# Optimization experiments

Measured on AMD Instinct MI355X. Metric: run time of the kernel, lower is better.

The kernel has to match this reference:

```python
import jax, jax.numpy as jnp
import numpy as np

FEAT_STRIDE = 8
SCALES = (4.0, 8.0, 16.0)
RATIOS = (0.5, 1.0, 2.0)
A = len(SCALES) * len(RATIOS)          # 9 anchors per location
PRE_NMS = 2048
POST_NMS = 300
NMS_THRESH = 0.7


def _gen_base_anchors():
    # cube anchors at scale*stride, ratio applied to depth; boxes (x1,y1,z1,x2,y2,z2)
    base = float(FEAT_STRIDE)
    ctr = (base - 1.0) / 2.0
    boxes = []
    for r in RATIOS:
        for s in SCALES:
            w = h = base * s
            d = base * s * r
            boxes.append([ctr - 0.5 * (w - 1), ctr - 0.5 * (h - 1), ctr - 0.5 * (d - 1),
                          ctr + 0.5 * (w - 1), ctr + 0.5 * (h - 1), ctr + 0.5 * (d - 1)])
    return jnp.asarray(boxes, jnp.float32)  # [A,6]


def _all_anchors(D, H, W):
    sz = jnp.arange(D, dtype=jnp.float32) * FEAT_STRIDE
    sy = jnp.arange(H, dtype=jnp.float32) * FEAT_STRIDE
    sx = jnp.arange(W, dtype=jnp.float32) * FEAT_STRIDE
    zz, yy, xx = jnp.meshgrid(sz, sy, sx, indexing='ij')  # order (d,h,w) matches score layout
    shifts = jnp.stack([xx, yy, zz, xx, yy, zz], -1).reshape(-1, 6)  # [K,6]
    return (shifts[:, None, :] + _gen_base_anchors()[None]).reshape(-1, 6)  # [K*A,6]


def _apply_deltas(anchors, deltas):
    w = anchors[:, 3] - anchors[:, 0] + 1.0
    h = anchors[:, 4] - anchors[:, 1] + 1.0
    d = anchors[:, 5] - anchors[:, 2] + 1.0
    cx = anchors[:, 0] + 0.5 * w
    cy = anchors[:, 1] + 0.5 * h
    cz = anchors[:, 2] + 0.5 * d
    dx, dy, dz, dw, dh, dd = [deltas[:, i] for i in range(6)]
    pcx = dx * w + cx; pcy = dy * h + cy; pcz = dz * d + cz
    pw = jnp.exp(dw) * w; ph = jnp.exp(dh) * h; pd = jnp.exp(dd) * d
    return jnp.stack([pcx - 0.5 * pw, pcy - 0.5 * ph, pcz - 0.5 * pd,
                      pcx + 0.5 * pw, pcy + 0.5 * ph, pcz + 0.5 * pd], -1)


def _clip_boxes(boxes, iminfo):  # iminfo = [D_im, H_im, W_im]
    lo = jnp.zeros((6,), boxes.dtype)
    hi = jnp.stack([iminfo[2], iminfo[1], iminfo[0], iminfo[2], iminfo[1], iminfo[0]]) - 1.0
    return jnp.clip(boxes, lo[None, :], hi[None, :])


def _pairwise_iou3d(b):  # b: [N,6]
    lo = jnp.maximum(b[:, None, :3], b[None, :, :3])          # [N,N,3]
    hi = jnp.minimum(b[:, None, 3:], b[None, :, 3:])
    inter = jnp.prod(jnp.clip(hi - lo + 1.0, 0.0), axis=-1)   # [N,N]
    vol = jnp.prod(b[:, 3:] - b[:, :3] + 1.0, axis=-1)        # [N]
    return inter / (vol[:, None] + vol[None, :] - inter)


def _nms_keep(iou):
    N = iou.shape[0]
    idx = jnp.arange(N)
    def body(i, keep):
        sup = (iou[i] > NMS_THRESH) & keep[i] & (idx > i)
        return keep & ~sup
    return jax.lax.fori_loop(0, N, body, jnp.ones((N,), bool))


def _propose_one(scores, deltas, anchors, iminfo):
    boxes = _clip_boxes(_apply_deltas(anchors, deltas), iminfo)  # [KA,6]
    _, order = jax.lax.top_k(scores, PRE_NMS)
    b = boxes[order]                                             # [PRE,6], score-sorted desc
    keep = _nms_keep(_pairwise_iou3d(b))
    key = jnp.where(keep, jnp.arange(PRE_NMS), PRE_NMS)
    sel = jnp.argsort(key)[:POST_NMS]                            # first POST_NMS kept, in score order
    valid = (key[sel] < PRE_NMS).astype(b.dtype)
    return b[sel] * valid[:, None]                               # zero-padded rows if < POST_NMS kept


def _forward(base_feat, im_info, W_conv, b_conv, W_cls, b_cls, W_bbox, b_bbox):
    B, C, D, H, W = base_feat.shape
    x = jax.lax.conv_general_dilated(
        base_feat, W_conv, (1, 1, 1), ((1, 1), (1, 1), (1, 1)),
        dimension_numbers=('NCDHW', 'OIDHW', 'NCDHW'))
    x = jax.nn.relu(x + b_conv[None, :, None, None, None])       # [B,512,D,H,W]
    cls = jnp.einsum('bcdhw,oc->bodhw', x, W_cls) + b_cls[None, :, None, None, None]
    prob = jax.nn.softmax(cls.reshape(B, 2, A, D, H, W), axis=1)  # reshape(x,2) + softmax(dim=1)
    fg = prob[:, 1]                                               # [B,A,D,H,W]
    scores = jnp.transpose(fg, (0, 2, 3, 4, 1)).reshape(B, -1)    # [B, K*A], order (d,h,w,a)
    bb = jnp.einsum('bcdhw,oc->bodhw', x, W_bbox) + b_bbox[None, :, None, None, None]
    deltas = jnp.transpose(bb.reshape(B, A, 6, D, H, W), (0, 3, 4, 5, 1, 2)).reshape(B, -1, 6)
    anchors = _all_anchors(D, H, W)
    rois6 = jax.vmap(lambda s, d, im: _propose_one(s, d, anchors, im))(scores, deltas, im_info)
    bidx = jnp.broadcast_to(jnp.arange(B, dtype=rois6.dtype)[:, None, None], (B, POST_NMS, 1))
    return jnp.concatenate([bidx, rois6], -1)                     # [B, POST_NMS, 7]


def setup_inputs() -> dict:
    key = jax.random.key(0)
    ks = jax.random.split(key, 4)
    B, din, D, H, W = 2, 128, 8, 32, 32
    base_feat = jax.random.normal(ks[0], (B, din, D, H, W), jnp.float32)
    im_info = jnp.asarray([[64.0, 256.0, 256.0]] * B, jnp.float32)  # (D_im, H_im, W_im)
    gt_boxes = jnp.zeros((B, 20, 7), jnp.float32)
    num_boxes = jnp.zeros((B,), jnp.int64)
    W_conv = jax.random.normal(ks[1], (512, din, 3, 3, 3), jnp.float32) * 0.02
    b_conv = jnp.zeros((512,), jnp.float32)
    W_cls = jax.random.normal(ks[2], (2 * A, 512), jnp.float32) * 0.01
    b_cls = jnp.zeros((2 * A,), jnp.float32)
    W_bbox = jax.random.normal(ks[3], (6 * A, 512), jnp.float32) * 0.01
    b_bbox = jnp.zeros((6 * A,), jnp.float32)
    return {"base_feat": base_feat, "im_info": im_info, "gt_boxes": gt_boxes,
            "num_boxes": num_boxes, "W_conv": W_conv, "b_conv": b_conv,
            "W_cls": W_cls, "b_cls": b_cls, "W_bbox": W_bbox, "b_bbox": b_bbox}


def reference(base_feat, im_info, gt_boxes, num_boxes, W_conv, b_conv, W_cls, b_cls, W_bbox, b_bbox):
    # Eval-mode RPN forward: losses are 0 in the original; gt_boxes/num_boxes unused.
    rois = _forward(base_feat, im_info, W_conv, b_conv, W_cls, b_cls, W_bbox, b_bbox)
    return rois
```

## Files before the change

kernel.cpp:

```cpp
#include <hip/hip_runtime.h>
#include <stdint.h>

#define BATCH 2
#define CIN 128
#define COUT 512
#define DD 8
#define PSPAT 8192
#define NA 9
#define NANCH 73728
#define PRE 2048
#define POST 300
#define CAP 4096
#define NMS_TH 0.7f

typedef unsigned short u16;
typedef _Float16 f16x8 __attribute__((ext_vector_type(8)));
typedef float f32x16 __attribute__((ext_vector_type(16)));
typedef unsigned int uint32x4 __attribute__((ext_vector_type(4)));

constexpr size_t OFF_WT   = 0;
constexpr size_t OFF_WHT  = 7077888;
constexpr size_t OFF_X    = 7241728;
constexpr size_t OFF_SC   = 40796160;
constexpr size_t OFF_BX   = 41385984;
constexpr size_t OFF_SB   = 44957696;
constexpr size_t OFF_MK   = 45056000;
constexpr size_t OFF_HIST = 16;
constexpr size_t OFF_CAND = 524304;

#define NT_WT   (27 * 128 * 512)
#define NT_WHT  (512 * 80)
__global__ void k_wtrans(const float* __restrict__ Wc, u16* __restrict__ Wg,
                         const float* __restrict__ Wcls, const float* __restrict__ Wbb,
                         float* __restrict__ Wht) {
    int e = blockIdx.x * blockDim.x + threadIdx.x;
    if (e < NT_WT) {
        const int k    = e & 63;
        const int n    = (e >> 6) & 127;
        const int half = (e >> 13) & 1;
        const int rest = e >> 14;
        const int co = (rest / 27) * 128 + n;
        const int ci = half * 64 + k;
        const int tp = rest % 27;
        const float v = Wc[(co * 128 + ci) * 27 + tp] * 1024.f;
        const _Float16 h = (_Float16)v;
        const _Float16 l = (_Float16)(v - (float)h);
        char* rb = (char*)Wg + (((size_t)(rest * 2 + half)) << 15) + n * 256;
        const int hcol = (k >> 3) ^ (n & 15);
        const int lcol = ((k >> 3) | 8) ^ (n & 15);
        const int kb = (k & 7) << 1;
        *(u16*)(rb + (hcol << 4) + kb) = __builtin_bit_cast(unsigned short, h);
        *(u16*)(rb + (lcol << 4) + kb) = __builtin_bit_cast(unsigned short, l);
        return;
    }
    e -= NT_WT;
    if (e >= NT_WHT) return;
    int q = e % 80;
    int c = e / 80;
    int og = q / 10, k = q % 10;
    int o = og * 9 + k;
    float v = 0.f;
    if (k < 9) v = (o < 18) ? Wcls[o * 512 + c] : Wbb[(o - 18) * 512 + c];
    Wht[e] = v;
}

#define MFMA(A, B, C) __builtin_amdgcn_mfma_f32_32x32x16_f16((A), (B), (C), 0, 0, 0)
#define Z16 {0.f,0.f,0.f,0.f,0.f,0.f,0.f,0.f,0.f,0.f,0.f,0.f,0.f,0.f,0.f,0.f}

#define PK2(YA, YB, UH, UL) { \
    const float sa_ = (YA) * 1024.f, sb_ = (YB) * 1024.f; \
    const _Float16 ha_ = (_Float16)sa_, hb_ = (_Float16)sb_; \
    const _Float16 la_ = (_Float16)(sa_ - (float)ha_); \
    const _Float16 lb_ = (_Float16)(sb_ - (float)hb_); \
    UH = (unsigned)__builtin_bit_cast(unsigned short, ha_) | \
         ((unsigned)__builtin_bit_cast(unsigned short, hb_) << 16); \
    UL = (unsigned)__builtin_bit_cast(unsigned short, la_) | \
         ((unsigned)__builtin_bit_cast(unsigned short, lb_) << 16); }

#define BLDI(N, KK) { \
    const int h2_ = hb_ + (N); \
    const bool ok_ = okw_ && ((unsigned)h2_ < 32u); \
    const float* ap_ = in + (((size_t)(cb0_ + ((KK) << 4))) << 13) + spo_ + (h2_ << 5); \
    y[N][KK][0] = ok_ ? ap_[0]     : 0.f; \
    y[N][KK][1] = ok_ ? ap_[8192]  : 0.f; \
    y[N][KK][2] = ok_ ? ap_[16384] : 0.f; \
    y[N][KK][3] = ok_ ? ap_[24576] : 0.f; \
    y[N][KK][4] = ok_ ? ap_[32768] : 0.f; \
    y[N][KK][5] = ok_ ? ap_[40960] : 0.f; \
    y[N][KK][6] = ok_ ? ap_[49152] : 0.f; \
    y[N][KK][7] = ok_ ? ap_[57344] : 0.f; }

#define ALOADISS(S) { \
    const int tap_ = t0 + ((S) >> 1); \
    const int kd_ = tap_ / 9, kh_ = (tap_ / 3) % 3, kw_ = tap_ % 3; \
    const int id_ = d0 + kd_ - 1; \
    const int w2_ = l31 + kw_ - 1; \
    const bool okw_ = (unsigned)w2_ < 32u; \
    const int hb_ = h0 + (wn << 1) + kh_ - 1; \
    const int cb0_ = b * CIN + (((S) & 1) << 6) + (cq << 3); \
    const long long spo_ = ((long long)id_ << 10) + w2_; \
    BLDI(0, 0) BLDI(0, 1) BLDI(0, 2) BLDI(0, 3) \
    BLDI(1, 0) BLDI(1, 1) BLDI(1, 2) BLDI(1, 3) }

#define CVTFRAG(N, KK, BH, BL) { \
    unsigned uh0_, uh1_, uh2_, uh3_, ul0_, ul1_, ul2_, ul3_; \
    PK2(y[N][KK][0], y[N][KK][1], uh0_, ul0_) \
    PK2(y[N][KK][2], y[N][KK][3], uh1_, ul1_) \
    PK2(y[N][KK][4], y[N][KK][5], uh2_, ul2_) \
    PK2(y[N][KK][6], y[N][KK][7], uh3_, ul3_) \
    { uint32x4 th_ = {uh0_, uh1_, uh2_, uh3_}; BH = __builtin_bit_cast(f16x8, th_); } \
    { uint32x4 tl_ = {ul0_, ul1_, ul2_, ul3_}; BL = __builtin_bit_cast(f16x8, tl_); } }

#define CVTALL() { \
    CVTFRAG(0, 0, bh00, bl00) CVTFRAG(0, 1, bh01, bl01) \
    CVTFRAG(0, 2, bh02, bl02) CVTFRAG(0, 3, bh03, bl03) \
    CVTFRAG(1, 0, bh10, bl10) CVTFRAG(1, 1, bh11, bl11) \
    CVTFRAG(1, 2, bh12, bl12) CVTFRAG(1, 3, bh13, bl13) }

#define WISSUE(S, BUF) { \
    const int tap_ = t0 + ((S) >> 1); \
    const char* gw_ = WgB + (((size_t)((nt * 27 + tap_) * 2 + ((S) & 1))) << 15) \
                    + (wv << 13) + ln16; \
    char* lb_ = smem + ((BUF) << 15) + (wv << 13); \
    _Pragma("unroll") \
    for (int j_ = 0; j_ < 8; ++j_) \
        __builtin_amdgcn_global_load_lds( \
            (const __attribute__((address_space(1))) void*)(gw_ + (j_ << 10)), \
            (__attribute__((address_space(3))) void*)(lb_ + (j_ << 10)), 16, 0, 0); }

#define KKSTEP(KK, BH0, BL0, BH1, BL1) { \
    const int ch_ = ((((KK) << 1) + cq) ^ rsw) << 4; \
    const int cl_ = (((((KK) << 1) + cq) | 8) ^ rsw) << 4; \
    const char* r0_ = wb_ + (rm0 << 8); \
    const char* r1_ = wb_ + (rm1 << 8); \
    const f16x8 wh0 = *(const f16x8*)(r0_ + ch_); \
    const f16x8 wl0 = *(const f16x8*)(r0_ + cl_); \
    const f16x8 wh1 = *(const f16x8*)(r1_ + ch_); \
    const f16x8 wl1 = *(const f16x8*)(r1_ + cl_); \
    acc00 = MFMA(wh0, BH0, acc00); acc00 = MFMA(wh0, BL0, acc00); acc00 = MFMA(wl0, BH0, acc00); \
    acc01 = MFMA(wh0, BH1, acc01); acc01 = MFMA(wh0, BL1, acc01); acc01 = MFMA(wl0, BH1, acc01); \
    acc10 = MFMA(wh1, BH0, acc10); acc10 = MFMA(wh1, BL0, acc10); acc10 = MFMA(wl1, BH0, acc10); \
    acc11 = MFMA(wh1, BH1, acc11); acc11 = MFMA(wh1, BL1, acc11); acc11 = MFMA(wl1, BH1, acc11); }

#define COMPUTE(BUF) { \
    const char* wb_ = smem + ((BUF) << 15); \
    KKSTEP(0, bh00, bl00, bh10, bl10) \
    KKSTEP(1, bh01, bl01, bh11, bl11) \
    KKSTEP(2, bh02, bl02, bh12, bl12) \
    KKSTEP(3, bh03, bl03, bh13, bl13) }

#define EPI(ACC, MI, NI) { \
    const int coB_ = co0 + (wm << 6) + ((MI) << 5) + hl4; \
    const int pt_  = p0 + (wn << 6) + ((NI) << 5) + l31; \
    _Pragma("unroll") \
    for (int g_ = 0; g_ < 4; ++g_) { \
        _Pragma("unroll") \
        for (int q_ = 0; q_ < 4; ++q_) { \
            const int co_ = coB_ + (g_ << 3) + q_; \
            const float v_ = ACC[g_ * 4 + q_] * 9.5367431640625e-07f + bconv[co_]; \
            x[((size_t)((b << 9) + co_) << 13) + pt_] = fmaxf(v_, 0.f); \
        } } }

__global__ __launch_bounds__(256, 2) void k_conv(const float* __restrict__ in,
                                                 const u16* __restrict__ Wg,
                                                 const float* __restrict__ bconv,
                                                 float* __restrict__ x) {
    __shared__ __align__(16) char smem[65536];
    const int tid  = threadIdx.x;
    const int bx   = blockIdx.x;
    const int nt   = blockIdx.y;
    const int b    = blockIdx.z;
    const int p0   = bx << 7;
    const int d0   = bx >> 3;
    const int h0   = (bx & 7) << 2;
    const int co0  = nt << 7;

    const int lane = tid & 63;
    const int wv   = tid >> 6;
    const int wm   = wv & 1;
    const int wn   = wv >> 1;
    const int l31  = lane & 31;
    const int cq   = lane >> 5;
    const int hl4  = cq << 2;
    const int rsw  = l31 & 15;
    const int rm0  = (wm << 6) + l31;
    const int rm1  = rm0 + 32;
    const int ln16 = lane << 4;

    const int t0   = (d0 == 0) ? 9 : 0;
    const int nTap = 27 - (((d0 == 0) || (d0 == 7)) ? 9 : 0);
    const int NS   = nTap * 2;

    const char* WgB = (const char*)Wg;

    float y[2][4][8];
    f16x8 bh00, bh01, bh02, bh03, bh10, bh11, bh12, bh13;
    f16x8 bl00, bl01, bl02, bl03, bl10, bl11, bl12, bl13;
    f32x16 acc00 = Z16, acc01 = Z16, acc10 = Z16, acc11 = Z16;

    WISSUE(0, 0)
    ALOADISS(0)
    __syncthreads();

    for (int s = 0; s < NS; ++s) {
        if (s + 1 < NS) { WISSUE(s + 1, (s + 1) & 1) }
        CVTALL()
        __builtin_amdgcn_sched_barrier(0);
        if (s + 1 < NS) { ALOADISS(s + 1) }
        __builtin_amdgcn_sched_barrier(0);
        COMPUTE(s & 1)
        __syncthreads();
    }

    EPI(acc00, 0, 0)
    EPI(acc01, 0, 1)
    EPI(acc10, 1, 0)
    EPI(acc11, 1, 1)
}

__global__ __launch_bounds__(256) void k_heads(const float* __restrict__ x,
                                               const float* __restrict__ Wht,
                                               const float* __restrict__ bcls,
                                               const float* __restrict__ bbb,
                                               const float* __restrict__ iminfo,
                                               float* __restrict__ scores,
                                               float* __restrict__ boxes,
                                               unsigned int* __restrict__ hist) {
    __shared__ __align__(16) float smx[4096];
    __shared__ __align__(16) float Whs[2560];
    __shared__ __align__(16) float ex[10240];
    const int tid = threadIdx.x;
    const int p0  = blockIdx.x * 128;
    const int b   = blockIdx.y;
    const int pl  = tid & 31;
    const int og  = tid >> 5;

    float acc[4][9] = {};

    for (int cc = 0; cc < 512; cc += 32) {
        __syncthreads();
        #pragma unroll
        for (int i = 0; i < 4; ++i) {
            int e4 = tid + i * 256;
            int ch = e4 >> 5;
            int pt4 = (e4 & 31) * 4;
            *(float4*)&smx[ch * 128 + pt4] =
                *(const float4*)&x[((size_t)(b * COUT + cc + ch) << 13) + p0 + pt4];
        }
        #pragma unroll
        for (int i = 0; i < 10; ++i) {
            int e = tid + i * 256;
            Whs[e] = Wht[cc * 80 + e];
        }
        __syncthreads();
        for (int kk = 0; kk < 32; ++kk) {
            float4 a4 = *(const float4*)&smx[kk * 128 + pl * 4];
            const float* wp = &Whs[kk * 80 + og * 10];
            float2 w0 = *(const float2*)(wp);
            float2 w1 = *(const float2*)(wp + 2);
            float2 w2 = *(const float2*)(wp + 4);
            float2 w3 = *(const float2*)(wp + 6);
            float  w8 = wp[8];
            float wv[9] = {w0.x, w0.y, w1.x, w1.y, w2.x, w2.y, w3.x, w3.y, w8};
            #pragma unroll
            for (int k = 0; k < 9; ++k) {
                float wk = wv[k];
                acc[0][k] += a4.x * wk;
                acc[1][k] += a4.y * wk;
                acc[2][k] += a4.z * wk;
                acc[3][k] += a4.w * wk;
            }
        }
    }

    __syncthreads();
    #pragma unroll
    for (int pi = 0; pi < 4; ++pi)
        #pragma unroll
        for (int k = 0; k < 9; ++k)
            ex[(pl * 4 + pi) * 80 + og * 10 + k] = acc[pi][k];
    __syncthreads();

    if (tid < 128) {
        const int p = p0 + tid;
        float v[72];
        #pragma unroll
        for (int og2 = 0; og2 < 8; ++og2)
            #pragma unroll
            for (int k = 0; k < 9; ++k)
                v[og2 * 9 + k] = ex[tid * 80 + og2 * 10 + k];

        const float im0 = iminfo[b * 3 + 0], im1 = iminfo[b * 3 + 1], im2 = iminfo[b * 3 + 2];
        const float hix = im2 - 1.f, hiy = im1 - 1.f, hiz = im0 - 1.f;
        const int d = p >> 10, h = (p >> 5) & 31, w = p & 31;
        const float sx = w * 8.f, sy = h * 8.f, sz = d * 8.f;

        #pragma unroll 1
        for (int a = 0; a < 9; ++a) {
            float c0 = v[a] + bcls[a];
            float c1 = v[9 + a] + bcls[9 + a];
            float m  = fmaxf(c0, c1);
            float e0 = expf(c0 - m), e1 = expf(c1 - m);
            float sc = e1 / (e0 + e1);
            scores[b * NANCH + p * 9 + a] = sc;
            atomicAdd(&hist[b * 65536 + (__float_as_uint(sc) >> 16)], 1u);

            float aw = (float)(32 << (a % 3));
            float ad = aw * 0.5f * (float)(1 << (a / 3));
            float ax1 = sx + 3.5f - 0.5f * (aw - 1.f);
            float ax2 = sx + 3.5f + 0.5f * (aw - 1.f);
            float ay1 = sy + 3.5f - 0.5f * (aw - 1.f);
            float ay2 = sy + 3.5f + 0.5f * (aw - 1.f);
            float az1 = sz + 3.5f - 0.5f * (ad - 1.f);
            float az2 = sz + 3.5f + 0.5f * (ad - 1.f);
            float ww_ = ax2 - ax1 + 1.f, hh_ = ay2 - ay1 + 1.f, dd_ = az2 - az1 + 1.f;
            float cx = ax1 + 0.5f * ww_, cy = ay1 + 0.5f * hh_, cz = az1 + 0.5f * dd_;

            const float* dv = &v[18 + a * 6];
            float dx = dv[0] + bbb[a * 6 + 0];
            float dy = dv[1] + bbb[a * 6 + 1];
            float dz = dv[2] + bbb[a * 6 + 2];
            float dw = dv[3] + bbb[a * 6 + 3];
            float dh = dv[4] + bbb[a * 6 + 4];
            float dd2 = dv[5] + bbb[a * 6 + 5];
            float pcx = dx * ww_ + cx, pcy = dy * hh_ + cy, pcz = dz * dd_ + cz;
            float pw = expf(dw) * ww_, ph = expf(dh) * hh_, pd = expf(dd2) * dd_;
            float x1 = fminf(fmaxf(pcx - 0.5f * pw, 0.f), hix);
            float y1 = fminf(fmaxf(pcy - 0.5f * ph, 0.f), hiy);
            float z1 = fminf(fmaxf(pcz - 0.5f * pd, 0.f), hiz);
            float x2 = fminf(fmaxf(pcx + 0.5f * pw, 0.f), hix);
            float y2 = fminf(fmaxf(pcy + 0.5f * ph, 0.f), hiy);
            float z2 = fminf(fmaxf(pcz + 0.5f * pd, 0.f), hiz);
            float* bp = &boxes[(size_t)(b * NANCH + p * 9 + a) * 6];
            bp[0] = x1; bp[1] = y1; bp[2] = z1; bp[3] = x2; bp[4] = y2; bp[5] = z2;
        }
    }
}

__global__ __launch_bounds__(1024) void k_cutcompact(const float* __restrict__ scores,
                                                     const unsigned int* __restrict__ hist,
                                                     unsigned long long* __restrict__ cand) {
    __shared__ unsigned int cs[1024], scan[1024];
    __shared__ unsigned int sh_cut, sh_pos;
    const int b = blockIdx.x, tid = threadIdx.x;
    const unsigned int* h = hist + b * 65536;
    unsigned int s = 0;
    for (int i = 0; i < 64; ++i) s += h[tid * 64 + i];
    cs[tid] = s; scan[tid] = s;
    if (tid == 0) sh_pos = 0;
    __syncthreads();
    for (int d = 1; d < 1024; d <<= 1) {
        unsigned int v = scan[tid];
        unsigned int add = (tid + d < 1024) ? scan[tid + d] : 0u;
        __syncthreads();
        scan[tid] = v + add;
        __syncthreads();
    }
    unsigned int above = (tid + 1 < 1024) ? scan[tid + 1] : 0u;
    if (above < PRE && above + cs[tid] >= PRE) {
        unsigned int cum = above;
        for (int x = tid * 64 + 63; x >= tid * 64; --x) {
            cum += h[x];
            if (cum >= PRE) { sh_cut = (unsigned int)x; break; }
        }
    }
    __syncthreads();
    const unsigned int cut = sh_cut;
    const float* sc = scores + b * NANCH;
    for (int i = tid; i < NANCH; i += 1024) {
        unsigned int u = __float_as_uint(sc[i]);
        if ((u >> 16) >= cut) {
            unsigned int pos = atomicAdd(&sh_pos, 1u);
            if (pos < CAP) cand[b * CAP + pos] = ((unsigned long long)(~u) << 32) | (unsigned)i;
        }
    }
    __syncthreads();
    const unsigned int cnt = (sh_pos < CAP) ? sh_pos : CAP;
    for (int i = (int)cnt + tid; i < CAP; i += 1024)
        cand[b * CAP + i] = ~0ull;
}

__global__ __launch_bounds__(1024) void k_sort2(const unsigned long long* __restrict__ cand,
                                                const float* __restrict__ boxes,
                                                float* __restrict__ sboxes) {
    __shared__ unsigned long long sk[CAP];
    const int b = blockIdx.x, tid = threadIdx.x;
    for (int i = tid; i < CAP; i += 1024) sk[i] = cand[b * CAP + i];
    __syncthreads();
    for (int k = 2; k <= CAP; k <<= 1) {
        for (int j = k >> 1; j > 0; j >>= 1) {
            #pragma unroll 1
            for (int i = tid; i < CAP; i += 1024) {
                int ixj = i ^ j;
                if (ixj > i) {
                    unsigned long long va = sk[i], vb = sk[ixj];
                    bool up = ((i & k) == 0);
                    if ((va > vb) == up) { sk[i] = vb; sk[ixj] = va; }
                }
            }
            __syncthreads();
        }
    }
    for (int r = tid; r < PRE; r += 1024) {
        unsigned int n = (unsigned int)(sk[r] & 0xFFFFFFFFull);
        const float* src = &boxes[(size_t)(b * NANCH + (int)n) * 6];
        float* dst = &sboxes[(size_t)(b * PRE + r) * 6];
        #pragma unroll
        for (int c = 0; c < 6; ++c) dst[c] = src[c];
    }
}

__global__ __launch_bounds__(256) void k_mask(const float* __restrict__ sboxes,
                                              unsigned long long* __restrict__ mask) {
    if (blockIdx.y < blockIdx.x) return;
    __shared__ float rb[64 * 6], cb[64 * 6];
    const int i0 = blockIdx.x * 64, j0 = blockIdx.y * 64, b = blockIdx.z;
    const int tid = threadIdx.x;
    for (int e = tid; e < 384; e += 256) {
        rb[e] = sboxes[(size_t)(b * PRE + i0) * 6 + e];
        cb[e] = sboxes[(size_t)(b * PRE + j0) * 6 + e];
    }
    __syncthreads();
    const int wave = tid >> 6, lane = tid & 63;
    const float bx1 = cb[lane * 6 + 0], by1 = cb[lane * 6 + 1], bz1 = cb[lane * 6 + 2];
    const float bx2 = cb[lane * 6 + 3], by2 = cb[lane * 6 + 4], bz2 = cb[lane * 6 + 5];
    const float vb = (bx2 - bx1 + 1.f) * (by2 - by1 + 1.f) * (bz2 - bz1 + 1.f);
    const int j = j0 + lane;
    for (int rr = 0; rr < 16; ++rr) {
        const int il = wave * 16 + rr;
        const int i = i0 + il;
        float ax1 = rb[il * 6 + 0], ay1 = rb[il * 6 + 1], az1 = rb[il * 6 + 2];
        float ax2 = rb[il * 6 + 3], ay2 = rb[il * 6 + 4], az2 = rb[il * 6 + 5];
        float va = (ax2 - ax1 + 1.f) * (ay2 - ay1 + 1.f) * (az2 - az1 + 1.f);
        float ix = fmaxf(fminf(ax2, bx2) - fmaxf(ax1, bx1) + 1.f, 0.f);
        float iy = fmaxf(fminf(ay2, by2) - fmaxf(ay1, by1) + 1.f, 0.f);
        float iz = fmaxf(fminf(az2, bz2) - fmaxf(az1, bz1) + 1.f, 0.f);
        float inter = ix * iy * iz;
        float iou = inter / (va + vb - inter);
        bool bit = (j > i) && (iou > NMS_TH);
        unsigned long long word = __ballot(bit);
        if (lane == 0) mask[(size_t)(b * PRE + i) * 32 + (j0 >> 6)] = word;
    }
}

__global__ __launch_bounds__(64) void k_nms(const unsigned long long* __restrict__ mask,
                                            const float* __restrict__ sboxes,
                                            float* __restrict__ out) {
    const int b = blockIdx.x, lane = threadIdx.x;
    __shared__ int sel[POST];
    unsigned long long keep = ~0ull;
    const int lw = lane & 31;
    const unsigned long long* mrow = mask + (size_t)b * PRE * 32 + lw;
    unsigned long long b0 = mrow[0 * 32], b1 = mrow[1 * 32], b2 = mrow[2 * 32], b3 = mrow[3 * 32];
    unsigned long long b4 = mrow[4 * 32], b5 = mrow[5 * 32], b6 = mrow[6 * 32], b7 = mrow[7 * 32];
    int kcount = 0;

#define NMS_STEP(J, BUF)                                                        \
    {                                                                           \
        int i = i0 + (J);                                                       \
        unsigned long long cur = (lw >= (i >> 6)) ? BUF : 0ull;                 \
        int nr = i0 + 8 + (J);                                                  \
        BUF = (nr < PRE) ? mrow[(size_t)nr * 32] : 0ull;                        \
        unsigned long long kw = __shfl(keep, i >> 6);                           \
        if ((kw >> (i & 63)) & 1ull) {                                          \
            if (lane < 32) keep &= ~cur;                                        \
            if (lane == 0 && kcount < POST) sel[kcount] = i;                    \
            ++kcount;                                                           \
            if (kcount >= POST) goto nms_done;                                  \
        }                                                                       \
    }

    for (int i0 = 0; i0 < PRE; i0 += 8) {
        NMS_STEP(0, b0) NMS_STEP(1, b1) NMS_STEP(2, b2) NMS_STEP(3, b3)
        NMS_STEP(4, b4) NMS_STEP(5, b5) NMS_STEP(6, b6) NMS_STEP(7, b7)
    }
nms_done:
    __syncthreads();
    const int kc = kcount;
    for (int r = lane; r < POST; r += 64) {
        float* op = &out[(size_t)(b * POST + r) * 7];
        op[0] = (float)b;
        if (r < kc) {
            const float* sb = &sboxes[(size_t)(b * PRE + sel[r]) * 6];
            #pragma unroll
            for (int c = 0; c < 6; ++c) op[1 + c] = sb[c];
        } else {
            #pragma unroll
            for (int c = 0; c < 6; ++c) op[1 + c] = 0.f;
        }
    }
#undef NMS_STEP
}

extern "C" void kernel_launch(void* const* d_in, const int* in_sizes, int n_in,
                              void* d_out, int out_size, void* d_ws, size_t ws_size,
                              hipStream_t stream) {
    const float* base_feat = (const float*)d_in[0];
    const float* im_info   = (const float*)d_in[1];
    const float* W_conv    = (const float*)d_in[4];
    const float* b_conv    = (const float*)d_in[5];
    const float* W_cls     = (const float*)d_in[6];
    const float* b_cls     = (const float*)d_in[7];
    const float* W_bbox    = (const float*)d_in[8];
    const float* b_bbox    = (const float*)d_in[9];

    char* ws = (char*)d_ws;
    u16* Wg        = (u16*)(ws + OFF_WT);
    float* Wht     = (float*)(ws + OFF_WHT);
    float* x       = (float*)(ws + OFF_X);
    float* scores  = (float*)(ws + OFF_SC);
    float* boxes   = (float*)(ws + OFF_BX);
    float* sboxes  = (float*)(ws + OFF_SB);
    unsigned long long* mask = (unsigned long long*)(ws + OFF_MK);
    unsigned int* hist = (unsigned int*)(ws + OFF_HIST);
    unsigned long long* cand = (unsigned long long*)(ws + OFF_CAND);

    const int NTRANS = NT_WT + NT_WHT;
    k_wtrans<<<(NTRANS + 255) / 256, 256, 0, stream>>>(W_conv, Wg, W_cls, W_bbox, Wht);
    k_conv<<<dim3(64, 4, 2), 256, 0, stream>>>(base_feat, Wg, b_conv, x);
    hipMemsetAsync(hist, 0, BATCH * 65536 * sizeof(unsigned int), stream);
    k_heads<<<dim3(64, 2), 256, 0, stream>>>(x, Wht, b_cls, b_bbox, im_info, scores, boxes, hist);
    k_cutcompact<<<BATCH, 1024, 0, stream>>>(scores, hist, cand);
    k_sort2<<<BATCH, 1024, 0, stream>>>(cand, boxes, sboxes);
    k_mask<<<dim3(32, 32, 2), 256, 0, stream>>>(sboxes, mask);
    k_nms<<<BATCH, 64, 0, stream>>>(mask, sboxes, (float*)d_out);
}
```

Measured before the change: 650.7 us.

## Pre-split input into channel-last fp16 hi/lo buffers for conv

Adds a pre-pass kernel that transposes the input to a channel-innermost layout and splits it into fp16 high and low halves once. The conv kernel then loads ready f16x8 fragments with vector loads instead of eight strided scalar fp32 loads plus per-fragment conversion, and double-buffers the A operands across steps. This removes the conversion work repeated across the four output-channel tiles and the uncoalesced loads. The cost is an extra launch and extra workspace traffic, and it falls back to the old kernel when the workspace is too small.

```diff
diff --git a/kernel.cpp b/kernel.cpp
--- a/kernel.cpp
+++ b/kernel.cpp
@@ -27,6 +27,9 @@
 constexpr size_t OFF_MK   = 45056000;
 constexpr size_t OFF_HIST = 16;
 constexpr size_t OFF_CAND = 524304;
+constexpr size_t OFF_XH   = 46104576;
+constexpr size_t OFF_XL   = 50298880;
+constexpr size_t WS_NEED_FAST = 54493184;
 
 #define NT_WT   (27 * 128 * 512)
 #define NT_WHT  (512 * 80)
@@ -64,58 +67,35 @@
     Wht[e] = v;
 }
 
+__global__ __launch_bounds__(256) void k_split(const float* __restrict__ in,
+                                               u16* __restrict__ xh, u16* __restrict__ xl) {
+    __shared__ float t[128][33];
+    const int blk = blockIdx.x;
+    const int b = blk >> 8, d = (blk >> 5) & 7, h = blk & 31;
+    const int tid = threadIdx.x;
+    const float* src = in + ((size_t)b << 20) + d * 1024 + h * 32;
+    #pragma unroll
+    for (int i = 0; i < 16; ++i) {
+        const int e = tid + i * 256;
+        const int ci = e >> 5, w = e & 31;
+        t[ci][w] = src[(size_t)ci * 8192 + w];
+    }
+    __syncthreads();
+    const size_t ob = (size_t)((b * 8 + d) * 32 + h) * 4096;
+    #pragma unroll
+    for (int i = 0; i < 16; ++i) {
+        const int e = tid + i * 256;
+        const int w = e >> 7, ci = e & 127;
+        const float v = t[ci][w] * 1024.f;
+        const _Float16 hh = (_Float16)v;
+        const _Float16 ll = (_Float16)(v - (float)hh);
+        xh[ob + w * 128 + ci] = __builtin_bit_cast(unsigned short, hh);
+        xl[ob + w * 128 + ci] = __builtin_bit_cast(unsigned short, ll);
+    }
+}
+
 #define MFMA(A, B, C) __builtin_amdgcn_mfma_f32_32x32x16_f16((A), (B), (C), 0, 0, 0)
 #define Z16 {0.f,0.f,0.f,0.f,0.f,0.f,0.f,0.f,0.f,0.f,0.f,0.f,0.f,0.f,0.f,0.f}
-
-#define PK2(YA, YB, UH, UL) { \
-    const float sa_ = (YA) * 1024.f, sb_ = (YB) * 1024.f; \
-    const _Float16 ha_ = (_Float16)sa_, hb_ = (_Float16)sb_; \
-    const _Float16 la_ = (_Float16)(sa_ - (float)ha_); \
-    const _Float16 lb_ = (_Float16)(sb_ - (float)hb_); \
-    UH = (unsigned)__builtin_bit_cast(unsigned short, ha_) | \
-         ((unsigned)__builtin_bit_cast(unsigned short, hb_) << 16); \
-    UL = (unsigned)__builtin_bit_cast(unsigned short, la_) | \
-         ((unsigned)__builtin_bit_cast(unsigned short, lb_) << 16); }
-
-#define BLDI(N, KK) { \
-    const int h2_ = hb_ + (N); \
-    const bool ok_ = okw_ && ((unsigned)h2_ < 32u); \
-    const float* ap_ = in + (((size_t)(cb0_ + ((KK) << 4))) << 13) + spo_ + (h2_ << 5); \
-    y[N][KK][0] = ok_ ? ap_[0]     : 0.f; \
-    y[N][KK][1] = ok_ ? ap_[8192]  : 0.f; \
-    y[N][KK][2] = ok_ ? ap_[16384] : 0.f; \
-    y[N][KK][3] = ok_ ? ap_[24576] : 0.f; \
-    y[N][KK][4] = ok_ ? ap_[32768] : 0.f; \
-    y[N][KK][5] = ok_ ? ap_[40960] : 0.f; \
-    y[N][KK][6] = ok_ ? ap_[49152] : 0.f; \
-    y[N][KK][7] = ok_ ? ap_[57344] : 0.f; }
-
-#define ALOADISS(S) { \
-    const int tap_ = t0 + ((S) >> 1); \
-    const int kd_ = tap_ / 9, kh_ = (tap_ / 3) % 3, kw_ = tap_ % 3; \
-    const int id_ = d0 + kd_ - 1; \
-    const int w2_ = l31 + kw_ - 1; \
-    const bool okw_ = (unsigned)w2_ < 32u; \
-    const int hb_ = h0 + (wn << 1) + kh_ - 1; \
-    const int cb0_ = b * CIN + (((S) & 1) << 6) + (cq << 3); \
-    const long long spo_ = ((long long)id_ << 10) + w2_; \
-    BLDI(0, 0) BLDI(0, 1) BLDI(0, 2) BLDI(0, 3) \
-    BLDI(1, 0) BLDI(1, 1) BLDI(1, 2) BLDI(1, 3) }
-
-#define CVTFRAG(N, KK, BH, BL) { \
-    unsigned uh0_, uh1_, uh2_, uh3_, ul0_, ul1_, ul2_, ul3_; \
-    PK2(y[N][KK][0], y[N][KK][1], uh0_, ul0_) \
-    PK2(y[N][KK][2], y[N][KK][3], uh1_, ul1_) \
-    PK2(y[N][KK][4], y[N][KK][5], uh2_, ul2_) \
-    PK2(y[N][KK][6], y[N][KK][7], uh3_, ul3_) \
-    { uint32x4 th_ = {uh0_, uh1_, uh2_, uh3_}; BH = __builtin_bit_cast(f16x8, th_); } \
-    { uint32x4 tl_ = {ul0_, ul1_, ul2_, ul3_}; BL = __builtin_bit_cast(f16x8, tl_); } }
-
-#define CVTALL() { \
-    CVTFRAG(0, 0, bh00, bl00) CVTFRAG(0, 1, bh01, bl01) \
-    CVTFRAG(0, 2, bh02, bl02) CVTFRAG(0, 3, bh03, bl03) \
-    CVTFRAG(1, 0, bh10, bl10) CVTFRAG(1, 1, bh11, bl11) \
-    CVTFRAG(1, 2, bh12, bl12) CVTFRAG(1, 3, bh13, bl13) }
 
 #define WISSUE(S, BUF) { \
     const int tap_ = t0 + ((S) >> 1); \
@@ -142,13 +122,6 @@
     acc10 = MFMA(wh1, BH0, acc10); acc10 = MFMA(wh1, BL0, acc10); acc10 = MFMA(wl1, BH0, acc10); \
     acc11 = MFMA(wh1, BH1, acc11); acc11 = MFMA(wh1, BL1, acc11); acc11 = MFMA(wl1, BH1, acc11); }
 
-#define COMPUTE(BUF) { \
-    const char* wb_ = smem + ((BUF) << 15); \
-    KKSTEP(0, bh00, bl00, bh10, bl10) \
-    KKSTEP(1, bh01, bl01, bh11, bl11) \
-    KKSTEP(2, bh02, bl02, bh12, bl12) \
-    KKSTEP(3, bh03, bl03, bh13, bl13) }
-
 #define EPI(ACC, MI, NI) { \
     const int coB_ = co0 + (wm << 6) + ((MI) << 5) + hl4; \
     const int pt_  = p0 + (wn << 6) + ((NI) << 5) + l31; \
@@ -160,6 +133,156 @@
             const float v_ = ACC[g_ * 4 + q_] * 9.5367431640625e-07f + bconv[co_]; \
             x[((size_t)((b << 9) + co_) << 13) + pt_] = fmaxf(v_, 0.f); \
         } } }
+
+#define FLD(N, KK, BH, BL) { \
+    const int h2_ = hb_ + (N); \
+    const bool ok_ = okw_ && ((unsigned)h2_ < 32u); \
+    const size_t ix_ = sbase_ + ((size_t)((h2_ & 31) << 5) << 7); \
+    const f16x8 vh_ = *(const f16x8*)(xh + ix_ + ((KK) << 4)); \
+    const f16x8 vl_ = *(const f16x8*)(xl + ix_ + ((KK) << 4)); \
+    BH = ok_ ? vh_ : fz8; \
+    BL = ok_ ? vl_ : fz8; }
+
+#define ALOADF(S, P) { \
+    const int tap_ = t0 + ((S) >> 1); \
+    const int kd_ = tap_ / 9, kh_ = (tap_ / 3) % 3, kw_ = tap_ % 3; \
+    const int id_ = d0 + kd_ - 1; \
+    const int w2_ = l31 + kw_ - 1; \
+    const bool okw_ = (unsigned)w2_ < 32u; \
+    const int hb_ = h0 + (wn << 1) + kh_ - 1; \
+    const int cio_ = (((S) & 1) << 6) + (cq << 3); \
+    const size_t sbase_ = (((size_t)((b << 3) + id_)) << 17) + ((w2_ & 31) << 7) + cio_; \
+    FLD(0, 0, P##h00, P##l00) FLD(0, 1, P##h01, P##l01) \
+    FLD(0, 2, P##h02, P##l02) FLD(0, 3, P##h03, P##l03) \
+    FLD(1, 0, P##h10, P##l10) FLD(1, 1, P##h11, P##l11) \
+    FLD(1, 2, P##h12, P##l12) FLD(1, 3, P##h13, P##l13) }
+
+#define COMPUTEF(BUF, P) { \
+    const char* wb_ = smem + ((BUF) << 15); \
+    KKSTEP(0, P##h00, P##l00, P##h10, P##l10) \
+    KKSTEP(1, P##h01, P##l01, P##h11, P##l11) \
+    KKSTEP(2, P##h02, P##l02, P##h12, P##l12) \
+    KKSTEP(3, P##h03, P##l03, P##h13, P##l13) }
+
+__global__ __launch_bounds__(256, 2) void k_conv_f(const u16* __restrict__ xh,
+                                                   const u16* __restrict__ xl,
+                                                   const u16* __restrict__ Wg,
+                                                   const float* __restrict__ bconv,
+                                                   float* __restrict__ x) {
+    __shared__ __align__(16) char smem[65536];
+    const int tid  = threadIdx.x;
+    const int bx   = blockIdx.x;
+    const int nt   = blockIdx.y;
+    const int b    = blockIdx.z;
+    const int p0   = bx << 7;
+    const int d0   = bx >> 3;
+    const int h0   = (bx & 7) << 2;
+    const int co0  = nt << 7;
+
+    const int lane = tid & 63;
+    const int wv   = tid >> 6;
+    const int wm   = wv & 1;
+    const int wn   = wv >> 1;
+    const int l31  = lane & 31;
+    const int cq   = lane >> 5;
+    const int hl4  = cq << 2;
+    const int rsw  = l31 & 15;
+    const int rm0  = (wm << 6) + l31;
+    const int rm1  = rm0 + 32;
+    const int ln16 = lane << 4;
+
+    const int t0   = (d0 == 0) ? 9 : 0;
+    const int nTap = 27 - (((d0 == 0) || (d0 == 7)) ? 9 : 0);
+    const int NS   = nTap * 2;
+
+    const char* WgB = (const char*)Wg;
+    const f16x8 fz8 = {(_Float16)0.f, (_Float16)0.f, (_Float16)0.f, (_Float16)0.f,
+                       (_Float16)0.f, (_Float16)0.f, (_Float16)0.f, (_Float16)0.f};
+
+    f16x8 Ah00, Al00, Ah01, Al01, Ah02, Al02, Ah03, Al03,
+          Ah10, Al10, Ah11, Al11, Ah12, Al12, Ah13, Al13;
+    f16x8 Bh00, Bl00, Bh01, Bl01, Bh02, Bl02, Bh03, Bl03,
+          Bh10, Bl10, Bh11, Bl11, Bh12, Bl12, Bh13, Bl13;
+    f32x16 acc00 = Z16, acc01 = Z16, acc10 = Z16, acc11 = Z16;
+
+    WISSUE(0, 0)
+    ALOADF(0, A)
+    __syncthreads();
+
+    for (int s = 0; s < NS; s += 2) {
+        WISSUE(s + 1, 1)
+        ALOADF(s + 1, B)
+        __builtin_amdgcn_sched_barrier(0);
+        COMPUTEF(0, A)
+        __syncthreads();
+        if (s + 2 < NS) { WISSUE(s + 2, 0) ALOADF(s + 2, A) }
+        __builtin_amdgcn_sched_barrier(0);
+        COMPUTEF(1, B)
+        __syncthreads();
+    }
+
+    EPI(acc00, 0, 0)
+    EPI(acc01, 0, 1)
+    EPI(acc10, 1, 0)
+    EPI(acc11, 1, 1)
+}
+
+#define PK2(YA, YB, UH, UL) { \
+    const float sa_ = (YA) * 1024.f, sb_ = (YB) * 1024.f; \
+    const _Float16 ha_ = (_Float16)sa_, hb_ = (_Float16)sb_; \
+    const _Float16 la_ = (_Float16)(sa_ - (float)ha_); \
+    const _Float16 lb_ = (_Float16)(sb_ - (float)hb_); \
+    UH = (unsigned)__builtin_bit_cast(unsigned short, ha_) | \
+         ((unsigned)__builtin_bit_cast(unsigned short, hb_) << 16); \
+    UL = (unsigned)__builtin_bit_cast(unsigned short, la_) | \
+         ((unsigned)__builtin_bit_cast(unsigned short, lb_) << 16); }
+
+#define BLDI(N, KK) { \
+    const int h2_ = hb_ + (N); \
+    const bool ok_ = okw_ && ((unsigned)h2_ < 32u); \
+    const float* ap_ = in + (((size_t)(cb0_ + ((KK) << 4))) << 13) + spo_ + (h2_ << 5); \
+    y[N][KK][0] = ok_ ? ap_[0]     : 0.f; \
+    y[N][KK][1] = ok_ ? ap_[8192]  : 0.f; \
+    y[N][KK][2] = ok_ ? ap_[16384] : 0.f; \
+    y[N][KK][3] = ok_ ? ap_[24576] : 0.f; \
+    y[N][KK][4] = ok_ ? ap_[32768] : 0.f; \
+    y[N][KK][5] = ok_ ? ap_[40960] : 0.f; \
+    y[N][KK][6] = ok_ ? ap_[49152] : 0.f; \
+    y[N][KK][7] = ok_ ? ap_[57344] : 0.f; }
+
+#define ALOADISS(S) { \
+    const int tap_ = t0 + ((S) >> 1); \
+    const int kd_ = tap_ / 9, kh_ = (tap_ / 3) % 3, kw_ = tap_ % 3; \
+    const int id_ = d0 + kd_ - 1; \
+    const int w2_ = l31 + kw_ - 1; \
+    const bool okw_ = (unsigned)w2_ < 32u; \
+    const int hb_ = h0 + (wn << 1) + kh_ - 1; \
+    const int cb0_ = b * CIN + (((S) & 1) << 6) + (cq << 3); \
+    const long long spo_ = ((long long)id_ << 10) + w2_; \
+    BLDI(0, 0) BLDI(0, 1) BLDI(0, 2) BLDI(0, 3) \
+    BLDI(1, 0) BLDI(1, 1) BLDI(1, 2) BLDI(1, 3) }
+
+#define CVTFRAG(N, KK, BH, BL) { \
+    unsigned uh0_, uh1_, uh2_, uh3_, ul0_, ul1_, ul2_, ul3_; \
+    PK2(y[N][KK][0], y[N][KK][1], uh0_, ul0_) \
+    PK2(y[N][KK][2], y[N][KK][3], uh1_, ul1_) \
+    PK2(y[N][KK][4], y[N][KK][5], uh2_, ul2_) \
+    PK2(y[N][KK][6], y[N][KK][7], uh3_, ul3_) \
+    { uint32x4 th_ = {uh0_, uh1_, uh2_, uh3_}; BH = __builtin_bit_cast(f16x8, th_); } \
+    { uint32x4 tl_ = {ul0_, ul1_, ul2_, ul3_}; BL = __builtin_bit_cast(f16x8, tl_); } }
+
+#define CVTALL() { \
+    CVTFRAG(0, 0, bh00, bl00) CVTFRAG(0, 1, bh01, bl01) \
+    CVTFRAG(0, 2, bh02, bl02) CVTFRAG(0, 3, bh03, bl03) \
+    CVTFRAG(1, 0, bh10, bl10) CVTFRAG(1, 1, bh11, bl11) \
+    CVTFRAG(1, 2, bh12, bl12) CVTFRAG(1, 3, bh13, bl13) }
+
+#define COMPUTE(BUF) { \
+    const char* wb_ = smem + ((BUF) << 15); \
+    KKSTEP(0, bh00, bl00, bh10, bl10) \
+    KKSTEP(1, bh01, bl01, bh11, bl11) \
+    KKSTEP(2, bh02, bl02, bh12, bl12) \
+    KKSTEP(3, bh03, bl03, bh13, bl13) }
 
 __global__ __launch_bounds__(256, 2) void k_conv(const float* __restrict__ in,
                                                  const u16* __restrict__ Wg,
@@ -514,10 +637,17 @@
     unsigned long long* mask = (unsigned long long*)(ws + OFF_MK);
     unsigned int* hist = (unsigned int*)(ws + OFF_HIST);
     unsigned long long* cand = (unsigned long long*)(ws + OFF_CAND);
+    u16* xh        = (u16*)(ws + OFF_XH);
+    u16* xl        = (u16*)(ws + OFF_XL);
 
     const int NTRANS = NT_WT + NT_WHT;
     k_wtrans<<<(NTRANS + 255) / 256, 256, 0, stream>>>(W_conv, Wg, W_cls, W_bbox, Wht);
-    k_conv<<<dim3(64, 4, 2), 256, 0, stream>>>(base_feat, Wg, b_conv, x);
+    if (ws_size >= WS_NEED_FAST) {
+        k_split<<<512, 256, 0, stream>>>(base_feat, xh, xl);
+        k_conv_f<<<dim3(64, 4, 2), 256, 0, stream>>>(xh, xl, Wg, b_conv, x);
+    } else {
+        k_conv<<<dim3(64, 4, 2), 256, 0, stream>>>(base_feat, Wg, b_conv, x);
+    }
     hipMemsetAsync(hist, 0, BATCH * 65536 * sizeof(unsigned int), stream);
     k_heads<<<dim3(64, 2), 256, 0, stream>>>(x, Wht, b_cls, b_bbox, im_info, scores, boxes, hist);
     k_cutcompact<<<BATCH, 1024, 0, stream>>>(scores, hist, cand);
```

After: 667.1 us. 2.5% more time.
